# Kernel optimization log

Hardware: AMD Instinct MI355X
Metric: run time of the kernel (lower is better)

Reference implementation:

```python
import jax, jax.numpy as jnp
import numpy as np

K = 31          # local attention window (odd)
PAD = (K - 1) // 2
G = 8           # heads / groups
MC = 48         # model_complexity (attention out_features)
OF = 88         # output_features
BN_EPS = 1e-5


def conv2d(x, w, b):
    # x: [B,C,H,W], w: [O,I,3,3], 'SAME' == padding=1 for stride-1 3x3
    y = jax.lax.conv_general_dilated(x, w, (1, 1), 'SAME',
                                     dimension_numbers=('NCHW', 'OIHW', 'NCHW'))
    return y + b[None, :, None, None]


def bn(x, g, b, m, v):
    # inference-mode BatchNorm2d over channel dim of NCHW
    return (x - m[None, :, None, None]) * (g[None, :, None, None] /
           jnp.sqrt(v[None, :, None, None] + BN_EPS)) + b[None, :, None, None]


def maxpool_w2(x):
    # MaxPool2d((1,2)): pool width (freq) by 2
    return jax.lax.reduce_window(x, -jnp.inf, jax.lax.max,
                                 (1, 1, 1, 2), (1, 1, 1, 2), 'VALID')


def setup_inputs() -> dict:
    key = jax.random.key(0)
    ks = jax.random.split(key, 24)
    B, T, F = 8, 2560, 229
    C1, C2 = OF // 16, OF // 8          # 5, 11
    freq_feats = C2 * (F // 2 // 2)      # 11 * 57 = 627
    s = lambda k, shp, sc=0.05: jax.random.normal(k, shp, dtype=jnp.float32) * sc
    inp = {
        'spec':   jax.random.normal(ks[0], (B, T, F), dtype=jnp.float32),
        'c1_w': s(ks[1], (C1, 1, 3, 3)),  'c1_b': s(ks[2], (C1,)),
        'bn1_g': jnp.ones((C1,)), 'bn1_b': jnp.zeros((C1,)),
        'bn1_m': jnp.zeros((C1,)), 'bn1_v': jnp.ones((C1,)),
        'c2_w': s(ks[3], (C1, C1, 3, 3)), 'c2_b': s(ks[4], (C1,)),
        'bn2_g': jnp.ones((C1,)), 'bn2_b': jnp.zeros((C1,)),
        'bn2_m': jnp.zeros((C1,)), 'bn2_v': jnp.ones((C1,)),
        'c3_w': s(ks[5], (C2, C1, 3, 3)), 'c3_b': s(ks[6], (C2,)),
        'bn3_g': jnp.ones((C2,)), 'bn3_b': jnp.zeros((C2,)),
        'bn3_m': jnp.zeros((C2,)), 'bn3_v': jnp.ones((C2,)),
        'fc_w': s(ks[7], (OF, freq_feats)), 'fc_b': s(ks[8], (OF,)),
        'wq': s(ks[9], (MC, OF)), 'wk': s(ks[10], (MC, OF)), 'wv': s(ks[11], (MC, OF)),
        'rel': jax.random.normal(ks[12], (1, MC, K), dtype=jnp.float32),
        'ln_g': jnp.ones((MC,)), 'ln_b': jnp.zeros((MC,)),
        'lin_w': s(ks[13], (OF, MC)), 'lin_b': s(ks[14], (OF,)),
    }
    return inp


def reference(spec, c1_w, c1_b, bn1_g, bn1_b, bn1_m, bn1_v,
              c2_w, c2_b, bn2_g, bn2_b, bn2_m, bn2_v,
              c3_w, c3_b, bn3_g, bn3_b, bn3_m, bn3_v,
              fc_w, fc_b, wq, wk, wv, rel, ln_g, ln_b, lin_w, lin_b):
    B, T, F = spec.shape
    # ---- ConvStack (eval mode: BN uses running stats, dropout = identity) ----
    x = spec[:, None]                                  # [B,1,T,F]
    x = jax.nn.relu(bn(conv2d(x, c1_w, c1_b), bn1_g, bn1_b, bn1_m, bn1_v))
    x = jax.nn.relu(bn(conv2d(x, c2_w, c2_b), bn2_g, bn2_b, bn2_m, bn2_v))
    x = maxpool_w2(x)                                  # F -> F//2
    x = jax.nn.relu(bn(conv2d(x, c3_w, c3_b), bn3_g, bn3_b, bn3_m, bn3_v))
    x = maxpool_w2(x)                                  # F//2 -> F//4
    x = jnp.transpose(x, (0, 2, 1, 3)).reshape(B, T, -1)  # [B,T,C2*(F//4)]
    x = x @ fc_w.T + fc_b                              # [B,T,OF]

    # ---- MutliHeadAttention1D: local windowed attention via unfold ----
    q = x @ wq.T                                       # [B,T,MC]
    xp = jnp.pad(x, ((0, 0), (PAD, PAD), (0, 0)))
    k = xp @ wk.T                                      # [B,T+K-1,MC]
    v = xp @ wv.T
    idx = jnp.arange(T)[:, None] + jnp.arange(K)[None, :]   # [T,K]
    kw = jnp.transpose(k[:, idx], (0, 1, 3, 2)) + rel        # [B,T,MC,K]
    vw = jnp.transpose(v[:, idx], (0, 1, 3, 2))              # [B,T,MC,K]
    Dh = MC // G
    kw = kw.reshape(B, T, G, Dh, K)
    vw = vw.reshape(B, T, G, Dh, K)
    qh = q.reshape(B, T, G, Dh, 1)
    energy = (qh * kw).sum(-2, keepdims=True)          # [B,T,G,1,K]
    attn = jax.nn.softmax(energy, axis=-1)
    out = (attn * vw).sum(-1).reshape(B, T, MC)        # [B,T,MC]
    a = attn.squeeze(3)                                # [B,T,G,K]

    # ---- LayerNorm + Linear + sigmoid ----
    mu = out.mean(-1, keepdims=True)
    var = jnp.mean((out - mu) ** 2, axis=-1, keepdims=True)
    h = (out - mu) / jnp.sqrt(var + 1e-5) * ln_g + ln_b
    frame_pred = jax.nn.sigmoid(h @ lin_w.T + lin_b)   # [B,T,OF]
    return frame_pred, a
```

## Files before the change

### kernel.cpp

```cpp
#include <hip/hip_runtime.h>
#include <hip/hip_bf16.h>
#include <math.h>

#define B_    8
#define T_    2560
#define F_    229
#define C1_   5
#define C2_   11
#define W1_   114
#define W2_   57
#define KP_   640
#define OF_   88
#define MC_   48
#define G_    8
#define DH_   6
#define K_    31
#define PAD_  15
#define BN_EPS 1e-5f
#define LN_EPS 1e-5f
#define TS_   8
#define TT_   16

typedef __attribute__((ext_vector_type(8))) short short8;
typedef __attribute__((ext_vector_type(4))) float f32x4;
typedef _Float16 h2 __attribute__((ext_vector_type(2)));

static inline int cdiv(int a, int b) { return (a + b - 1) / b; }

union H2U { h2 h; unsigned u; };

__device__ inline h2 uph2(unsigned u) { H2U x; x.u = u; return x.h; }
__device__ inline unsigned packh2(float lo, float hi) {
    H2U x;
    x.h.x = (_Float16)lo;
    x.h.y = (_Float16)hi;
    return x.u;
}

#if __has_builtin(__builtin_amdgcn_fdot2)
#define FDOT2(a, b, c) __builtin_amdgcn_fdot2((a), (b), (c), false)
#else
__device__ inline float FDOT2(h2 a, h2 b, float c) {
    return fmaf((float)a.x, (float)b.x, fmaf((float)a.y, (float)b.y, c));
}
#endif

__global__ __launch_bounds__(640, 8) void conv123_kernel(
        const float* __restrict__ spec,
        const float* __restrict__ c1w, const float* __restrict__ c1b,
        const float* __restrict__ g1, const float* __restrict__ b1,
        const float* __restrict__ m1, const float* __restrict__ v1,
        const float* __restrict__ c2w, const float* __restrict__ c2b,
        const float* __restrict__ g2, const float* __restrict__ b2,
        const float* __restrict__ m2, const float* __restrict__ v2,
        const float* __restrict__ c3w, const float* __restrict__ c3b,
        const float* __restrict__ g3, const float* __restrict__ b3,
        const float* __restrict__ m3, const float* __restrict__ v3,
        __hip_bfloat16* __restrict__ x3out) {
    __shared__ ushort x1t[12 * 5 * 232];
    __shared__ float specx2[14 * 232];
    __shared__ float w1s[45];
    __shared__ unsigned w2p[300];
    __shared__ unsigned w3p[660];
    __shared__ float scl1[5], shf1[5], scl2[5], shf2[5], scl3[11], shf3[11];
    int t0 = blockIdx.x * TS_;
    int b = blockIdx.y;
    int tid = threadIdx.x;

    if (tid < 45) w1s[tid] = c1w[tid];
    for (int i = tid; i < 75; i += 640) {
        int r = i % 15;
        const float* wp = c2w + (i / 15) * 45 + (r / 3) * 9 + (r % 3) * 3;
        float w0 = wp[0], w1 = wp[1], w2 = wp[2];
        unsigned* dst = &w2p[i * 4];
        dst[0] = packh2(w0, w1);
        dst[1] = packh2(w2, 0.f);
        dst[2] = packh2(0.f, w0);
        dst[3] = packh2(w1, w2);
    }
    for (int i = tid; i < 165; i += 640) {
        int r = i % 15;
        const float* wp = c3w + (i / 15) * 45 + (r / 3) * 9 + (r % 3) * 3;
        float w0 = wp[0], w1 = wp[1], w2 = wp[2];
        unsigned* dst = &w3p[i * 4];
        dst[0] = packh2(w0, w1);
        dst[1] = packh2(w2, 0.f);
        dst[2] = packh2(0.f, w0);
        dst[3] = packh2(w1, w2);
    }
    if (tid < 5) {
        float s = g1[tid] * rsqrtf(v1[tid] + BN_EPS);
        scl1[tid] = s;
        shf1[tid] = (c1b[tid] - m1[tid]) * s + b1[tid];
    }
    if (tid >= 64 && tid < 69) {
        int c = tid - 64;
        float s = g2[c] * rsqrtf(v2[c] + BN_EPS);
        scl2[c] = s;
        shf2[c] = (c2b[c] - m2[c]) * s + b2[c];
    }
    if (tid >= 128 && tid < 139) {
        int c = tid - 128;
        float s = g3[c] * rsqrtf(v3[c] + BN_EPS);
        scl3[c] = s;
        shf3[c] = (c3b[c] - m3[c]) * s + b3[c];
    }
    {
        const float* sb = spec + (size_t)b * T_ * F_;
        for (int i = tid; i < 14 * 232; i += 640) {
            int col = i % 232;
            int rr = i / 232;
            int t = t0 - 3 + rr;
            int f = col - 1;
            float v = 0.f;
            if (t >= 0 && t < T_ && f >= 0 && f < F_) v = sb[(size_t)t * F_ + f];
            specx2[i] = v;
        }
    }
    __syncthreads();

    for (int i = tid; i < 12 * 229; i += 640) {
        int f = i % 229;
        int rr = i / 229;
        int t = t0 - 2 + rr;
        float y[5];
        if (t >= 0 && t < T_) {
            float tp[9];
#pragma unroll
            for (int dt = 0; dt < 3; ++dt) {
                const float* row = &specx2[(rr + dt) * 232 + f];
                tp[dt * 3 + 0] = row[0];
                tp[dt * 3 + 1] = row[1];
                tp[dt * 3 + 2] = row[2];
            }
#pragma unroll
            for (int co = 0; co < 5; ++co) {
                float acc = 0.f;
#pragma unroll
                for (int k = 0; k < 9; ++k) acc = fmaf(tp[k], w1s[co * 9 + k], acc);
                y[co] = fmaxf(fmaf(acc, scl1[co], shf1[co]), 0.f);
            }
        } else {
#pragma unroll
            for (int co = 0; co < 5; ++co) y[co] = 0.f;
        }
#pragma unroll
        for (int co = 0; co < 5; ++co) {
            _Float16 h = (_Float16)y[co];
            x1t[(rr * 5 + co) * 232 + 1 + f] = *(ushort*)&h;
        }
    }
    for (int i = tid; i < 180; i += 640) {
        int c = i % 3;
        int col = (c == 0) ? 0 : 229 + c;
        int ci = (i / 3) % 5;
        int rr = i / 15;
        x1t[(rr * 5 + ci) * 232 + col] = 0;
    }
    __syncthreads();

    ushort* x2pt = (ushort*)specx2;
    if (tid < 570) {
        int co = tid / 114;
        int j = tid % 114;
        float acc0[10], acc1[10];
#pragma unroll
        for (int r = 0; r < 10; ++r) { acc0[r] = 0.f; acc1[r] = 0.f; }
#pragma unroll
        for (int ci = 0; ci < 5; ++ci) {
            const unsigned* wb = &w2p[(co * 5 + ci) * 12];
            h2 wA[3], wB[3], wC[3], wD[3];
#pragma unroll
            for (int dt = 0; dt < 3; ++dt) {
                wA[dt] = uph2(wb[dt * 4 + 0]);
                wB[dt] = uph2(wb[dt * 4 + 1]);
                wC[dt] = uph2(wb[dt * 4 + 2]);
                wD[dt] = uph2(wb[dt * 4 + 3]);
            }
#pragma unroll
            for (int rr = 0; rr < 12; ++rr) {
                const ushort* p = &x1t[(rr * 5 + ci) * 232 + 2 * j];
                unsigned u0 = *(const unsigned*)p;
                unsigned u1 = *(const unsigned*)(p + 2);
                h2 a0 = uph2(u0), a1 = uph2(u1);
#pragma unroll
                for (int dt = 0; dt < 3; ++dt) {
                    int r = rr - dt;
                    if (r >= 0 && r < 10) {
                        acc0[r] = FDOT2(a1, wB[dt], FDOT2(a0, wA[dt], acc0[r]));
                        acc1[r] = FDOT2(a1, wD[dt], FDOT2(a0, wC[dt], acc1[r]));
                    }
                }
            }
        }
        float s = scl2[co], sh = shf2[co];
        float yv[10];
#pragma unroll
        for (int r = 0; r < 10; ++r) {
            int t = t0 - 1 + r;
            float y = fmaxf(fmaxf(acc0[r] * s + sh, 0.f), fmaxf(acc1[r] * s + sh, 0.f));
            yv[r] = (t < 0 || t >= T_) ? 0.f : y;
        }
        __syncthreads();
#pragma unroll
        for (int r = 0; r < 10; ++r) {
            _Float16 h = (_Float16)yv[r];
            x2pt[(r * 5 + co) * 120 + 1 + j] = *(ushort*)&h;
        }
    } else {
        __syncthreads();
        for (int i = tid - 570; i < 300; i += 70) {
            int cc = i % 6;
            int col = (cc == 0) ? 0 : 114 + cc;
            int ci = (i / 6) % 5;
            int r = i / 30;
            x2pt[(r * 5 + ci) * 120 + col] = 0;
        }
    }
    __syncthreads();

    if (tid < 627) {
        int co = tid / 57;
        int j = tid % 57;
        float acc0[8], acc1[8];
#pragma unroll
        for (int r = 0; r < 8; ++r) { acc0[r] = 0.f; acc1[r] = 0.f; }
#pragma unroll
        for (int ci = 0; ci < 5; ++ci) {
            const unsigned* wb = &w3p[(co * 5 + ci) * 12];
            h2 wA[3], wB[3], wC[3], wD[3];
#pragma unroll
            for (int dt = 0; dt < 3; ++dt) {
                wA[dt] = uph2(wb[dt * 4 + 0]);
                wB[dt] = uph2(wb[dt * 4 + 1]);
                wC[dt] = uph2(wb[dt * 4 + 2]);
                wD[dt] = uph2(wb[dt * 4 + 3]);
            }
#pragma unroll
            for (int rr = 0; rr < 10; ++rr) {
                const ushort* p = &x2pt[(rr * 5 + ci) * 120 + 2 * j];
                unsigned u0 = *(const unsigned*)p;
                unsigned u1 = *(const unsigned*)(p + 2);
                h2 a0 = uph2(u0), a1 = uph2(u1);
#pragma unroll
                for (int dt = 0; dt < 3; ++dt) {
                    int r = rr - dt;
                    if (r >= 0 && r < 8) {
                        acc0[r] = FDOT2(a1, wB[dt], FDOT2(a0, wA[dt], acc0[r]));
                        acc1[r] = FDOT2(a1, wD[dt], FDOT2(a0, wC[dt], acc1[r]));
                    }
                }
            }
        }
        float s = scl3[co], sh = shf3[co];
#pragma unroll
        for (int r = 0; r < 8; ++r) {
            float y0 = fmaxf(acc0[r] * s + sh, 0.f);
            float y1 = fmaxf(acc1[r] * s + sh, 0.f);
            x3out[(size_t)(b * T_ + t0 + r) * KP_ + co * 57 + j] =
                __float2bfloat16(fmaxf(y0, y1));
        }
    } else if (tid >= 627 && tid < 640) {
        __hip_bfloat16 z = __float2bfloat16(0.f);
#pragma unroll
        for (int r = 0; r < 8; ++r)
            x3out[(size_t)(b * T_ + t0 + r) * KP_ + tid] = z;
    }
}

__global__ __launch_bounds__(256) void wprime_kernel(const float* __restrict__ fc_w,
        const float* __restrict__ fc_b, const float* __restrict__ wq,
        const float* __restrict__ wk, const float* __restrict__ wv,
        __hip_bfloat16* __restrict__ wp, float* __restrict__ bp) {
    int idx = blockIdx.x * 256 + threadIdx.x;
    if (idx < 144 * KP_) {
        int o = idx / KP_;
        int kk = idx % KP_;
        const float* Wrow = (o < 48) ? (wq + o * 88)
                          : (o < 96) ? (wk + (o - 48) * 88) : (wv + (o - 96) * 88);
        float s = 0.f;
        if (kk < 627)
            for (int i = 0; i < 88; ++i) s = fmaf(Wrow[i], fc_w[(size_t)i * 627 + kk], s);
        wp[idx] = __float2bfloat16(s);
    } else if (idx < 144 * KP_ + 144) {
        int o = idx - 144 * KP_;
        const float* Wrow = (o < 48) ? (wq + o * 88)
                          : (o < 96) ? (wk + (o - 48) * 88) : (wv + (o - 96) * 88);
        float s = 0.f;
        for (int i = 0; i < 88; ++i) s = fmaf(Wrow[i], fc_b[i], s);
        bp[o] = s;
    }
}

__global__ __launch_bounds__(256) void fc_qkv_mfma_kernel(
        const __hip_bfloat16* __restrict__ X, const __hip_bfloat16* __restrict__ Wp,
        const float* __restrict__ bp, float* __restrict__ Q) {
    int tid = threadIdx.x;
    int lane = tid & 63;
    int gw = blockIdx.x * 4 + (tid >> 6);
    int mtile = gw / 3;
    int nthird = gw % 3;
    const short* Xs = (const short*)X;
    const short* Ws = (const short*)Wp;
    int klane = (lane >> 4) * 8;
    const short* xrow = Xs + (size_t)(mtile * 16 + (lane & 15)) * KP_ + klane;
    const short* wrow = Ws + (size_t)(nthird * 48 + (lane & 15)) * KP_ + klane;
    f32x4 acc0 = {0.f, 0.f, 0.f, 0.f}, acc1 = acc0, acc2 = acc0;
#pragma unroll 4
    for (int kt = 0; kt < 20; ++kt) {
        short8 a = *(const short8*)(xrow + kt * 32);
        short8 b0 = *(const short8*)(wrow + kt * 32);
        short8 b1 = *(const short8*)(wrow + 16 * KP_ + kt * 32);
        short8 b2 = *(const short8*)(wrow + 32 * KP_ + kt * 32);
        acc0 = __builtin_amdgcn_mfma_f32_16x16x32_bf16(a, b0, acc0, 0, 0, 0);
        acc1 = __builtin_amdgcn_mfma_f32_16x16x32_bf16(a, b1, acc1, 0, 0, 0);
        acc2 = __builtin_amdgcn_mfma_f32_16x16x32_bf16(a, b2, acc2, 0, 0, 0);
    }
    int r0 = mtile * 16 + (lane >> 4) * 4;
    int col = lane & 15;
    f32x4 accs[3] = {acc0, acc1, acc2};
#pragma unroll
    for (int nt = 0; nt < 3; ++nt) {
        int o = nthird * 48 + nt * 16 + col;
        float bias = bp[o];
#pragma unroll
        for (int rg = 0; rg < 4; ++rg)
            Q[(size_t)(r0 + rg) * 144 + o] = accs[nt][rg] + bias;
    }
}

__global__ __launch_bounds__(256) void attn_ln_kernel(const float* __restrict__ Q,
        const float* __restrict__ rel, const float* __restrict__ lng,
        const float* __restrict__ lnb, const float* __restrict__ lw,
        const float* __restrict__ lb, float* __restrict__ fp,
        float* __restrict__ aout) {
    __shared__ float smem[6088];
    __shared__ float mus[TT_], rss[TT_];
    float* kvt = smem;
    float* relT = smem + 4600;
    int b = blockIdx.y;
    int t0 = blockIdx.x * TT_;
    int tid = threadIdx.x;
    int h = tid & 1;
    int p = tid >> 1;
    int g = p & 7;
    int tl = p >> 3;
    for (int i = tid; i < 46 * 48; i += 256) {
        int row = i / 48, c2 = i % 48;
        int t = t0 - 15 + row;
        float2 v = {0.f, 0.f};
        if (t >= 0 && t < T_)
            v = *(const float2*)&Q[((size_t)b * T_ + t) * 144 + 48 + 2 * c2];
        *(float2*)&kvt[row * 100 + 2 * c2] = v;
    }
    for (int i = tid; i < 31 * 48; i += 256) {
        int kp = i / 48, j = i % 48;
        relT[i] = rel[j * 31 + kp];
    }
    const float* qg = &Q[((size_t)b * T_ + t0 + tl) * 144 + g * 6];
    float2 q01 = *(const float2*)qg;
    float2 q23 = *(const float2*)(qg + 2);
    float2 q45 = *(const float2*)(qg + 4);
    __syncthreads();
    float e[16];
    float m_h = -1e30f;
#pragma unroll
    for (int i = 0; i < 16; ++i) {
        int kp = 2 * i + h;
        if (kp < 31) {
            const float* kr = &kvt[(tl + kp) * 100 + g * 6];
            const float* rr = &relT[kp * 48 + g * 6];
            float2 k01 = *(const float2*)kr;
            float2 k23 = *(const float2*)(kr + 2);
            float2 k45 = *(const float2*)(kr + 4);
            float2 r01 = *(const float2*)rr;
            float2 r23 = *(const float2*)(rr + 2);
            float2 r45 = *(const float2*)(rr + 4);
            float s = fmaf(q01.x, k01.x + r01.x,
                      fmaf(q01.y, k01.y + r01.y,
                      fmaf(q23.x, k23.x + r23.x,
                      fmaf(q23.y, k23.y + r23.y,
                      fmaf(q45.x, k45.x + r45.x,
                           q45.y * (k45.y + r45.y))))));
            e[i] = s;
            m_h = fmaxf(m_h, s);
        }
    }
    float M = fmaxf(m_h, __shfl_xor(m_h, 1));
    float s_h = 0.f;
    float o0 = 0, o1 = 0, o2 = 0, o3 = 0, o4 = 0, o5 = 0;
#pragma unroll
    for (int i = 0; i < 16; ++i) {
        int kp = 2 * i + h;
        if (kp < 31) {
            float a = __expf(e[i] - M);
            e[i] = a;
            s_h += a;
            const float* vr = &kvt[(tl + kp) * 100 + 48 + g * 6];
            float2 v01 = *(const float2*)vr;
            float2 v23 = *(const float2*)(vr + 2);
            float2 v45 = *(const float2*)(vr + 4);
            o0 = fmaf(a, v01.x, o0); o1 = fmaf(a, v01.y, o1);
            o2 = fmaf(a, v23.x, o2); o3 = fmaf(a, v23.y, o3);
            o4 = fmaf(a, v45.x, o4); o5 = fmaf(a, v45.y, o5);
        }
    }
    float sum = s_h + __shfl_xor(s_h, 1);
    float inv = 1.f / sum;
    float t0s = o0 + __shfl_xor(o0, 1);
    float t1s = o1 + __shfl_xor(o1, 1);
    float t2s = o2 + __shfl_xor(o2, 1);
    float t3s = o3 + __shfl_xor(o3, 1);
    float t4s = o4 + __shfl_xor(o4, 1);
    float t5s = o5 + __shfl_xor(o5, 1);
    __syncthreads();
    float* abuf = smem;
    float* xr = smem + 3968;
#pragma unroll
    for (int i = 0; i < 16; ++i) {
        int kp = 2 * i + h;
        if (kp < 31) abuf[p * 31 + kp] = e[i] * inv;
    }
    if (h == 0) {
        float* xp = &xr[tl * 48 + g * 6];
        xp[0] = t0s * inv; xp[1] = t1s * inv; xp[2] = t2s * inv;
        xp[3] = t3s * inv; xp[4] = t4s * inv; xp[5] = t5s * inv;
    }
    __syncthreads();
    size_t base = ((size_t)b * T_ + t0) * 248;
    for (int i = tid; i < 992; i += 256) {
        float4 v = *(const float4*)&abuf[4 * i];
        *(float4*)&aout[base + 4 * i] = v;
    }
    if (tid < TT_) {
        const float* row = &xr[tid * 48];
        float s = 0.f;
        for (int c = 0; c < 48; ++c) s += row[c];
        float mu = s * (1.f / 48.f);
        float v2 = 0.f;
        for (int c = 0; c < 48; ++c) { float d = row[c] - mu; v2 = fmaf(d, d, v2); }
        mus[tid] = mu;
        rss[tid] = rsqrtf(v2 * (1.f / 48.f) + LN_EPS);
    }
    __syncthreads();
    for (int i = tid; i < TT_ * 48; i += 256) {
        int r = i / 48, c = i % 48;
        xr[i] = fmaf((xr[i] - mus[r]) * rss[r], lng[c], lnb[c]);
    }
    __syncthreads();
    size_t obase = ((size_t)b * T_ + t0) * 88;
    for (int i = tid; i < TT_ * 88; i += 256) {
        int o = i % 88, r = i / 88;
        const float* xp = &xr[r * 48];
        const float* wpp = &lw[o * 48];
        float s = lb[o];
#pragma unroll
        for (int c = 0; c < 48; c += 4) {
            float4 xv = *(const float4*)&xp[c];
            float4 wv = *(const float4*)&wpp[c];
            s = fmaf(xv.x, wv.x, s);
            s = fmaf(xv.y, wv.y, s);
            s = fmaf(xv.z, wv.z, s);
            s = fmaf(xv.w, wv.w, s);
        }
        fp[obase + i] = 1.f / (1.f + __expf(-s));
    }
}

extern "C" void kernel_launch(void* const* d_in, const int* in_sizes, int n_in,
                              void* d_out, int out_size, void* d_ws, size_t ws_size,
                              hipStream_t stream) {
    const float* spec = (const float*)d_in[0];
    const float* c1_w = (const float*)d_in[1];
    const float* c1_b = (const float*)d_in[2];
    const float* bn1_g = (const float*)d_in[3];
    const float* bn1_b = (const float*)d_in[4];
    const float* bn1_m = (const float*)d_in[5];
    const float* bn1_v = (const float*)d_in[6];
    const float* c2_w = (const float*)d_in[7];
    const float* c2_b = (const float*)d_in[8];
    const float* bn2_g = (const float*)d_in[9];
    const float* bn2_b = (const float*)d_in[10];
    const float* bn2_m = (const float*)d_in[11];
    const float* bn2_v = (const float*)d_in[12];
    const float* c3_w = (const float*)d_in[13];
    const float* c3_b = (const float*)d_in[14];
    const float* bn3_g = (const float*)d_in[15];
    const float* bn3_b = (const float*)d_in[16];
    const float* bn3_m = (const float*)d_in[17];
    const float* bn3_v = (const float*)d_in[18];
    const float* fc_w = (const float*)d_in[19];
    const float* fc_b = (const float*)d_in[20];
    const float* wq = (const float*)d_in[21];
    const float* wk = (const float*)d_in[22];
    const float* wv = (const float*)d_in[23];
    const float* rel = (const float*)d_in[24];
    const float* ln_g = (const float*)d_in[25];
    const float* ln_b = (const float*)d_in[26];
    const float* lin_w = (const float*)d_in[27];
    const float* lin_b = (const float*)d_in[28];

    float* ws = (float*)d_ws;
    __hip_bfloat16* x3bf = (__hip_bfloat16*)ws;
    __hip_bfloat16* wp_bf = (__hip_bfloat16*)(ws + 19000000);
    float* bp = ws + 19100000;
    float* Qb = ws + 23449600;

    float* frame_pred = (float*)d_out;
    float* a_out = frame_pred + (size_t)B_ * T_ * OF_;

    wprime_kernel<<<cdiv(144 * KP_ + 144, 256), 256, 0, stream>>>(fc_w, fc_b, wq, wk, wv,
                                                                  wp_bf, bp);
    conv123_kernel<<<dim3(T_ / TS_, B_), 640, 0, stream>>>(
        spec, c1_w, c1_b, bn1_g, bn1_b, bn1_m, bn1_v,
        c2_w, c2_b, bn2_g, bn2_b, bn2_m, bn2_v,
        c3_w, c3_b, bn3_g, bn3_b, bn3_m, bn3_v, x3bf);
    fc_qkv_mfma_kernel<<<960, 256, 0, stream>>>(x3bf, wp_bf, bp, Qb);
    attn_ln_kernel<<<dim3(T_ / TT_, B_), 256, 0, stream>>>(Qb, rel, ln_g, ln_b, lin_w,
                                                           lin_b, frame_pred, a_out);
}
```

Before: 317.5 us.

## Register-tile conv stack with packed fp16 dot products and larger time tiles

Doubles the time tile per block to 16 rows, which lowers the share of halo recomputation. The first conv now runs on fp16 packed dot2 instructions over an fp16 copy of the spectrogram instead of scalar fp32 FMAs. All three conv stages are rebuilt so each thread computes a register tile of several rows and four to eight columns from vectorized 16-byte LDS loads, reusing each loaded input across rows. The trade-offs are fp16 precision on the raw input, more registers per thread (occupancy hint lowered from 8 to 5), and larger shared-memory buffers.

```diff
diff --git a/kernel.cpp b/kernel.cpp
--- a/kernel.cpp
+++ b/kernel.cpp
@@ -18,12 +18,13 @@
 #define PAD_  15
 #define BN_EPS 1e-5f
 #define LN_EPS 1e-5f
-#define TS_   8
+#define TS_   16
 #define TT_   16
 
 typedef __attribute__((ext_vector_type(8))) short short8;
 typedef __attribute__((ext_vector_type(4))) float f32x4;
 typedef _Float16 h2 __attribute__((ext_vector_type(2)));
+typedef __fp16 fp16x2 __attribute__((ext_vector_type(2)));
 
 static inline int cdiv(int a, int b) { return (a + b - 1) / b; }
 
@@ -37,6 +38,16 @@
     return x.u;
 }
 
+#if __has_builtin(__builtin_amdgcn_cvt_pkrtz)
+__device__ inline unsigned pkrtz(float a, float b) {
+    union { fp16x2 v; unsigned u; } x;
+    x.v = __builtin_amdgcn_cvt_pkrtz(a, b);
+    return x.u;
+}
+#else
+__device__ inline unsigned pkrtz(float a, float b) { return packh2(a, b); }
+#endif
+
 #if __has_builtin(__builtin_amdgcn_fdot2)
 #define FDOT2(a, b, c) __builtin_amdgcn_fdot2((a), (b), (c), false)
 #else
@@ -45,7 +56,7 @@
 }
 #endif
 
-__global__ __launch_bounds__(640, 8) void conv123_kernel(
+__global__ __launch_bounds__(640, 5) void conv123_kernel(
         const float* __restrict__ spec,
         const float* __restrict__ c1w, const float* __restrict__ c1b,
         const float* __restrict__ g1, const float* __restrict__ b1,
@@ -57,36 +68,42 @@
         const float* __restrict__ g3, const float* __restrict__ b3,
         const float* __restrict__ m3, const float* __restrict__ v3,
         __hip_bfloat16* __restrict__ x3out) {
-    __shared__ ushort x1t[12 * 5 * 232];
-    __shared__ float specx2[14 * 232];
-    __shared__ float w1s[45];
-    __shared__ unsigned w2p[300];
-    __shared__ unsigned w3p[660];
+    __shared__ __align__(16) ushort x1t[100 * 240];
+    __shared__ __align__(16) ushort x2u[10816];
+    __shared__ __align__(16) unsigned w1p[60];
+    __shared__ __align__(16) unsigned w2p[300];
+    __shared__ __align__(16) unsigned w3p[660];
     __shared__ float scl1[5], shf1[5], scl2[5], shf2[5], scl3[11], shf3[11];
     int t0 = blockIdx.x * TS_;
     int b = blockIdx.y;
     int tid = threadIdx.x;
 
-    if (tid < 45) w1s[tid] = c1w[tid];
+    if (tid < 15) {
+        int co = tid / 3, dt = tid % 3;
+        const float* wp = c1w + co * 9 + dt * 3;
+        unsigned* dst = &w1p[tid * 4];
+        dst[0] = packh2(wp[0], wp[1]);
+        dst[1] = packh2(wp[2], 0.f);
+        dst[2] = packh2(0.f, wp[0]);
+        dst[3] = packh2(wp[1], wp[2]);
+    }
     for (int i = tid; i < 75; i += 640) {
         int r = i % 15;
         const float* wp = c2w + (i / 15) * 45 + (r / 3) * 9 + (r % 3) * 3;
-        float w0 = wp[0], w1 = wp[1], w2 = wp[2];
         unsigned* dst = &w2p[i * 4];
-        dst[0] = packh2(w0, w1);
-        dst[1] = packh2(w2, 0.f);
-        dst[2] = packh2(0.f, w0);
-        dst[3] = packh2(w1, w2);
+        dst[0] = packh2(wp[0], wp[1]);
+        dst[1] = packh2(wp[2], 0.f);
+        dst[2] = packh2(0.f, wp[0]);
+        dst[3] = packh2(wp[1], wp[2]);
     }
     for (int i = tid; i < 165; i += 640) {
         int r = i % 15;
         const float* wp = c3w + (i / 15) * 45 + (r / 3) * 9 + (r % 3) * 3;
-        float w0 = wp[0], w1 = wp[1], w2 = wp[2];
         unsigned* dst = &w3p[i * 4];
-        dst[0] = packh2(w0, w1);
-        dst[1] = packh2(w2, 0.f);
-        dst[2] = packh2(0.f, w0);
-        dst[3] = packh2(w1, w2);
+        dst[0] = packh2(wp[0], wp[1]);
+        dst[1] = packh2(wp[2], 0.f);
+        dst[2] = packh2(0.f, wp[0]);
+        dst[3] = packh2(wp[1], wp[2]);
     }
     if (tid < 5) {
         float s = g1[tid] * rsqrtf(v1[tid] + BN_EPS);
@@ -107,164 +124,212 @@
     }
     {
         const float* sb = spec + (size_t)b * T_ * F_;
-        for (int i = tid; i < 14 * 232; i += 640) {
-            int col = i % 232;
-            int rr = i / 232;
-            int t = t0 - 3 + rr;
-            int f = col - 1;
-            float v = 0.f;
-            if (t >= 0 && t < T_ && f >= 0 && f < F_) v = sb[(size_t)t * F_ + f];
-            specx2[i] = v;
-        }
-    }
-    __syncthreads();
-
-    for (int i = tid; i < 12 * 229; i += 640) {
-        int f = i % 229;
-        int rr = i / 229;
-        int t = t0 - 2 + rr;
-        float y[5];
-        if (t >= 0 && t < T_) {
-            float tp[9];
+        for (int i = tid; i < 22 * 120; i += 640) {
+            int row = i / 120;
+            int pr = i - row * 120;
+            int t = t0 - 3 + row;
+            int c = 2 * pr - 4;
+            float va = 0.f, vb = 0.f;
+            if (t >= 0 && t < T_) {
+                const float* rp = sb + (size_t)t * F_;
+                if ((unsigned)c < 229u) va = rp[c];
+                if ((unsigned)(c + 1) < 229u) vb = rp[c + 1];
+            }
+            *(unsigned*)&x2u[row * 240 + 2 * pr] = packh2(va, vb);
+        }
+        if (tid == 0) { uint4 z = {0u, 0u, 0u, 0u}; *(uint4*)&x2u[10800] = z; }
+    }
+    __syncthreads();
+
+    if (tid < 580) {
+        int co = tid / 116;
+        int rem = tid - co * 116;
+        int q = rem >> 2;
+        int rg = rem & 3;
+        int rlo = rg * 5;
+        const unsigned* wb = &w1p[co * 12];
+        uint4 wv0 = *(const uint4*)wb;
+        uint4 wv1 = *(const uint4*)(wb + 4);
+        uint4 wv2 = *(const uint4*)(wb + 8);
+        h2 A1[3] = {uph2(wv0.x), uph2(wv1.x), uph2(wv2.x)};
+        h2 B1[3] = {uph2(wv0.y), uph2(wv1.y), uph2(wv2.y)};
+        h2 C1v[3] = {uph2(wv0.z), uph2(wv1.z), uph2(wv2.z)};
+        h2 D1[3] = {uph2(wv0.w), uph2(wv1.w), uph2(wv2.w)};
+        h2 X[7][5];
+        const ushort* sp = x2u + 8 * q;
+#pragma unroll
+        for (int s = 0; s < 7; ++s) {
+            const ushort* p = sp + (rlo + s) * 240;
+            uint4 xq = *(const uint4*)p;
+            unsigned xr = *(const unsigned*)(p + 8);
+            X[s][0] = uph2(xq.x); X[s][1] = uph2(xq.y);
+            X[s][2] = uph2(xq.z); X[s][3] = uph2(xq.w);
+            X[s][4] = uph2(xr);
+        }
+        float s1 = scl1[co], h1 = shf1[co];
+        int c0 = 8 * q - 3;
+#pragma unroll
+        for (int k = 0; k < 5; ++k) {
+            int rr1 = rlo + k;
+            int t = t0 - 2 + rr1;
+            bool vt = (t >= 0 && t < T_);
+            float y[8] = {0.f, 0.f, 0.f, 0.f, 0.f, 0.f, 0.f, 0.f};
 #pragma unroll
             for (int dt = 0; dt < 3; ++dt) {
-                const float* row = &specx2[(rr + dt) * 232 + f];
-                tp[dt * 3 + 0] = row[0];
-                tp[dt * 3 + 1] = row[1];
-                tp[dt * 3 + 2] = row[2];
-            }
-#pragma unroll
-            for (int co = 0; co < 5; ++co) {
-                float acc = 0.f;
-#pragma unroll
-                for (int k = 0; k < 9; ++k) acc = fmaf(tp[k], w1s[co * 9 + k], acc);
-                y[co] = fmaxf(fmaf(acc, scl1[co], shf1[co]), 0.f);
-            }
-        } else {
-#pragma unroll
-            for (int co = 0; co < 5; ++co) y[co] = 0.f;
-        }
-#pragma unroll
-        for (int co = 0; co < 5; ++co) {
-            _Float16 h = (_Float16)y[co];
-            x1t[(rr * 5 + co) * 232 + 1 + f] = *(ushort*)&h;
-        }
-    }
-    for (int i = tid; i < 180; i += 640) {
-        int c = i % 3;
-        int col = (c == 0) ? 0 : 229 + c;
-        int ci = (i / 3) % 5;
-        int rr = i / 15;
-        x1t[(rr * 5 + ci) * 232 + col] = 0;
-    }
-    __syncthreads();
-
-    ushort* x2pt = (ushort*)specx2;
-    if (tid < 570) {
-        int co = tid / 114;
-        int j = tid % 114;
-        float acc0[10], acc1[10];
-#pragma unroll
-        for (int r = 0; r < 10; ++r) { acc0[r] = 0.f; acc1[r] = 0.f; }
-#pragma unroll
+#pragma unroll
+                for (int l = 0; l < 4; ++l) {
+                    y[2 * l] = FDOT2(X[k + dt][l + 1], B1[dt],
+                               FDOT2(X[k + dt][l], A1[dt], y[2 * l]));
+                    y[2 * l + 1] = FDOT2(X[k + dt][l + 1], D1[dt],
+                                   FDOT2(X[k + dt][l], C1v[dt], y[2 * l + 1]));
+                }
+            }
+            unsigned pk[4];
+#pragma unroll
+            for (int m = 0; m < 4; ++m) {
+                float ya = fmaxf(fmaf(y[2 * m], s1, h1), 0.f);
+                float yb = fmaxf(fmaf(y[2 * m + 1], s1, h1), 0.f);
+                ya = (vt && (c0 + 2 * m) >= 0) ? ya : 0.f;
+                yb = (vt && (c0 + 2 * m + 1) >= 0) ? yb : 0.f;
+                pk[m] = pkrtz(ya, yb);
+            }
+            uint4 pw = {pk[0], pk[1], pk[2], pk[3]};
+            *(uint4*)&x1t[(rr1 * 5 + co) * 240 + 8 * q] = pw;
+        }
+    }
+    if (tid < 100) {
+        uint4 z = {0u, 0u, 0u, 0u};
+        *(uint4*)&x1t[tid * 240 + 232] = z;
+    }
+    __syncthreads();
+
+    if (tid < 580) {
+        int co = tid / 116;
+        int rem = tid - co * 116;
+        int q2 = rem >> 2;
+        int rg = rem & 3;
+        int rlo = rg * 4 + (rg ? 1 : 0);
+        float aE[5][4], aO[5][4];
+#pragma unroll
+        for (int i = 0; i < 5; ++i)
+#pragma unroll
+            for (int l = 0; l < 4; ++l) { aE[i][l] = 0.f; aO[i][l] = 0.f; }
+        const ushort* px = x1t + 8 * q2;
         for (int ci = 0; ci < 5; ++ci) {
             const unsigned* wb = &w2p[(co * 5 + ci) * 12];
-            h2 wA[3], wB[3], wC[3], wD[3];
-#pragma unroll
-            for (int dt = 0; dt < 3; ++dt) {
-                wA[dt] = uph2(wb[dt * 4 + 0]);
-                wB[dt] = uph2(wb[dt * 4 + 1]);
-                wC[dt] = uph2(wb[dt * 4 + 2]);
-                wD[dt] = uph2(wb[dt * 4 + 3]);
-            }
-#pragma unroll
-            for (int rr = 0; rr < 12; ++rr) {
-                const ushort* p = &x1t[(rr * 5 + ci) * 232 + 2 * j];
-                unsigned u0 = *(const unsigned*)p;
-                unsigned u1 = *(const unsigned*)(p + 2);
-                h2 a0 = uph2(u0), a1 = uph2(u1);
+            uint4 wv0 = *(const uint4*)wb;
+            uint4 wv1 = *(const uint4*)(wb + 4);
+            uint4 wv2 = *(const uint4*)(wb + 8);
+            h2 A[3] = {uph2(wv0.x), uph2(wv1.x), uph2(wv2.x)};
+            h2 Bb[3] = {uph2(wv0.y), uph2(wv1.y), uph2(wv2.y)};
+            h2 Cc[3] = {uph2(wv0.z), uph2(wv1.z), uph2(wv2.z)};
+            h2 Dd[3] = {uph2(wv0.w), uph2(wv1.w), uph2(wv2.w)};
+#pragma unroll
+            for (int k = 0; k < 7; ++k) {
+                const ushort* p = px + ((rlo + k) * 5 + ci) * 240;
+                uint4 xq = *(const uint4*)p;
+                unsigned xr = *(const unsigned*)(p + 8);
+                h2 X[5] = {uph2(xq.x), uph2(xq.y), uph2(xq.z), uph2(xq.w), uph2(xr)};
 #pragma unroll
                 for (int dt = 0; dt < 3; ++dt) {
-                    int r = rr - dt;
-                    if (r >= 0 && r < 10) {
-                        acc0[r] = FDOT2(a1, wB[dt], FDOT2(a0, wA[dt], acc0[r]));
-                        acc1[r] = FDOT2(a1, wD[dt], FDOT2(a0, wC[dt], acc1[r]));
+                    int lr = k - dt;
+                    if (lr >= 0 && lr < 5) {
+#pragma unroll
+                        for (int l = 0; l < 4; ++l) {
+                            aE[lr][l] = FDOT2(X[l + 1], Bb[dt],
+                                        FDOT2(X[l], A[dt], aE[lr][l]));
+                            aO[lr][l] = FDOT2(X[l + 1], Dd[dt],
+                                        FDOT2(X[l], Cc[dt], aO[lr][l]));
+                        }
                     }
                 }
             }
         }
         float s = scl2[co], sh = shf2[co];
-        float yv[10];
-#pragma unroll
-        for (int r = 0; r < 10; ++r) {
+#pragma unroll
+        for (int lr = 0; lr < 5; ++lr) {
+            int r = rlo + lr;
             int t = t0 - 1 + r;
-            float y = fmaxf(fmaxf(acc0[r] * s + sh, 0.f), fmaxf(acc1[r] * s + sh, 0.f));
-            yv[r] = (t < 0 || t >= T_) ? 0.f : y;
-        }
-        __syncthreads();
-#pragma unroll
-        for (int r = 0; r < 10; ++r) {
-            _Float16 h = (_Float16)yv[r];
-            x2pt[(r * 5 + co) * 120 + 1 + j] = *(ushort*)&h;
-        }
-    } else {
-        __syncthreads();
-        for (int i = tid - 570; i < 300; i += 70) {
-            int cc = i % 6;
-            int col = (cc == 0) ? 0 : 114 + cc;
-            int ci = (i / 6) % 5;
-            int r = i / 30;
-            x2pt[(r * 5 + ci) * 120 + col] = 0;
-        }
-    }
-    __syncthreads();
-
-    if (tid < 627) {
-        int co = tid / 57;
-        int j = tid % 57;
-        float acc0[8], acc1[8];
-#pragma unroll
-        for (int r = 0; r < 8; ++r) { acc0[r] = 0.f; acc1[r] = 0.f; }
-#pragma unroll
+            bool vt = (t >= 0 && t < T_);
+            float yv[4];
+#pragma unroll
+            for (int l = 0; l < 4; ++l) {
+                int j = 4 * q2 - 1 + l;
+                float y = fmaxf(fmaxf(fmaf(aE[lr][l], s, sh), 0.f),
+                                fmaxf(fmaf(aO[lr][l], s, sh), 0.f));
+                yv[l] = (vt && j >= 0 && j < 114) ? y : 0.f;
+            }
+            uint2 pw;
+            pw.x = pkrtz(yv[0], yv[1]);
+            pw.y = pkrtz(yv[2], yv[3]);
+            *(uint2*)&x2u[(r * 5 + co) * 120 + 4 * q2] = pw;
+        }
+    }
+    __syncthreads();
+
+    if (tid < 495) {
+        int co = tid / 45;
+        int rem = tid - co * 45;
+        int pq = rem / 3;
+        int rg = rem - pq * 3;
+        int rlo = rg * 5;
+        float aE[6][4], aO[6][4];
+#pragma unroll
+        for (int i = 0; i < 6; ++i)
+#pragma unroll
+            for (int l = 0; l < 4; ++l) { aE[i][l] = 0.f; aO[i][l] = 0.f; }
+        const ushort* px = x2u + 8 * pq;
         for (int ci = 0; ci < 5; ++ci) {
             const unsigned* wb = &w3p[(co * 5 + ci) * 12];
-            h2 wA[3], wB[3], wC[3], wD[3];
-#pragma unroll
-            for (int dt = 0; dt < 3; ++dt) {
-                wA[dt] = uph2(wb[dt * 4 + 0]);
-                wB[dt] = uph2(wb[dt * 4 + 1]);
-                wC[dt] = uph2(wb[dt * 4 + 2]);
-                wD[dt] = uph2(wb[dt * 4 + 3]);
-            }
-#pragma unroll
-            for (int rr = 0; rr < 10; ++rr) {
-                const ushort* p = &x2pt[(rr * 5 + ci) * 120 + 2 * j];
-                unsigned u0 = *(const unsigned*)p;
-                unsigned u1 = *(const unsigned*)(p + 2);
-                h2 a0 = uph2(u0), a1 = uph2(u1);
+            uint4 wv0 = *(const uint4*)wb;
+            uint4 wv1 = *(const uint4*)(wb + 4);
+            uint4 wv2 = *(const uint4*)(wb + 8);
+            h2 A[3] = {uph2(wv0.x), uph2(wv1.x), uph2(wv2.x)};
+            h2 Bb[3] = {uph2(wv0.y), uph2(wv1.y), uph2(wv2.y)};
+            h2 Cc[3] = {uph2(wv0.z), uph2(wv1.z), uph2(wv2.z)};
+            h2 Dd[3] = {uph2(wv0.w), uph2(wv1.w), uph2(wv2.w)};
+#pragma unroll
+            for (int k = 0; k < 8; ++k) {
+                const ushort* p = px + ((rlo + k) * 5 + ci) * 120;
+                uint4 xq = *(const uint4*)p;
+                unsigned xr = *(const unsigned*)(p + 8);
+                h2 X[5] = {uph2(xq.x), uph2(xq.y), uph2(xq.z), uph2(xq.w), uph2(xr)};
 #pragma unroll
                 for (int dt = 0; dt < 3; ++dt) {
-                    int r = rr - dt;
-                    if (r >= 0 && r < 8) {
-                        acc0[r] = FDOT2(a1, wB[dt], FDOT2(a0, wA[dt], acc0[r]));
-                        acc1[r] = FDOT2(a1, wD[dt], FDOT2(a0, wC[dt], acc1[r]));
+                    int lr = k - dt;
+                    if (lr >= 0 && lr < 6) {
+#pragma unroll
+                        for (int l = 0; l < 4; ++l) {
+                            aE[lr][l] = FDOT2(X[l + 1], Bb[dt],
+                                        FDOT2(X[l], A[dt], aE[lr][l]));
+                            aO[lr][l] = FDOT2(X[l + 1], Dd[dt],
+                                        FDOT2(X[l], Cc[dt], aO[lr][l]));
+                        }
                     }
                 }
             }
         }
         float s = scl3[co], sh = shf3[co];
 #pragma unroll
-        for (int r = 0; r < 8; ++r) {
-            float y0 = fmaxf(acc0[r] * s + sh, 0.f);
-            float y1 = fmaxf(acc1[r] * s + sh, 0.f);
-            x3out[(size_t)(b * T_ + t0 + r) * KP_ + co * 57 + j] =
-                __float2bfloat16(fmaxf(y0, y1));
-        }
-    } else if (tid >= 627 && tid < 640) {
+        for (int lr = 0; lr < 6; ++lr) {
+            int rout = rlo + lr;
+            size_t rowbase = (size_t)(b * T_ + t0 + rout) * KP_ + co * 57;
+#pragma unroll
+            for (int l = 0; l < 4; ++l) {
+                int j = 4 * pq + l;
+                if (j < 57) {
+                    float y = fmaxf(fmaxf(fmaf(aE[lr][l], s, sh), 0.f),
+                                    fmaxf(fmaf(aO[lr][l], s, sh), 0.f));
+                    x3out[rowbase + j] = __float2bfloat16(y);
+                }
+            }
+        }
+    } else {
         __hip_bfloat16 z = __float2bfloat16(0.f);
-#pragma unroll
-        for (int r = 0; r < 8; ++r)
-            x3out[(size_t)(b * T_ + t0 + r) * KP_ + tid] = z;
+        for (int i = tid - 495; i < 16 * 13; i += 145) {
+            int r = i / 13, c = 627 + (i - (i / 13) * 13);
+            x3out[(size_t)(b * T_ + t0 + r) * KP_ + c] = z;
+        }
     }
 }
 
```

Result: faster. 305.3 us (-3.8%).
